# Performance work log

Hardware: AMD Instinct MI355X
Metric: run time of the kernel (lower is better)

Reference implementation:

```python
import jax, jax.numpy as jnp
import numpy as np

BETA, ALPHA, NS_STEPS = 0.9, 1.0, 1
D_MODEL, D_STATE, D_CONV, EXPAND = 768, 16, 4, 2
D_INNER = EXPAND * D_MODEL
DT_RANK = -(-D_MODEL // 16)  # ceil(d_model/16) = 48
B, L = 2, 1024


def setup_inputs() -> dict:
    key = jax.random.key(0)
    ks = jax.random.split(key, 8)
    s = lambda k, shape, sc=0.02: jax.random.normal(k, shape, jnp.float32) * sc
    return {
        "hidden_states": jax.random.normal(ks[0], (B, L, D_MODEL), jnp.float32),
        "in_proj_w": s(ks[1], (2 * D_INNER, D_MODEL)),
        "conv_w": s(ks[2], (D_INNER, 1, D_CONV), 0.2),
        "conv_b": jnp.zeros((D_INNER,), jnp.float32),
        "x_proj_w": s(ks[3], (DT_RANK + 2 * D_STATE, D_INNER)),
        "dt_head_w": s(ks[4], (D_INNER, DT_RANK)),
        "dt_head_b": s(ks[5], (D_INNER,), 0.1),
        "out_proj_w": s(ks[6], (D_MODEL, D_INNER)),
        "D": jnp.ones((D_INNER,), jnp.float32),
    }


def _newton_schulz(G, steps):
    """Muon-style quintic Newton-Schulz orthogonalization of (b, d, n) with d >= n."""
    a, b, c = 3.4445, -4.7750, 2.0315
    X = G / (jnp.linalg.norm(G, axis=(-2, -1), keepdims=True) + 1e-7)
    X = X.swapaxes(-2, -1)  # (b, n, d): rows <= cols
    for _ in range(steps):
        A = X @ X.swapaxes(-2, -1)       # (b, n, n) small Gram
        Bm = b * A + c * (A @ A)
        X = a * X + Bm @ X
    return X.swapaxes(-2, -1)            # back to (b, d, n)


def reference(hidden_states, in_proj_w, conv_w, conv_b, x_proj_w, dt_head_w, dt_head_b, out_proj_w, D):
    Bz, Lz, _ = hidden_states.shape
    dtype = hidden_states.dtype
    # input projection -> x, z  (B, L, d_inner) each
    xz = jnp.einsum('bld,ed->ble', hidden_states, in_proj_w)
    x, z = jnp.split(xz, 2, axis=-1)
    # causal depthwise conv over time + SiLU
    xc = jax.lax.conv_general_dilated(
        x.swapaxes(1, 2), conv_w, (1,), [(D_CONV - 1, 0)],
        dimension_numbers=('NCH', 'OIH', 'NCH'), feature_group_count=D_INNER)
    x = jax.nn.silu(xc.swapaxes(1, 2) + conv_b)  # (B, L, d_inner)
    # projections for dt / k / q
    x_dbl = jnp.einsum('bld,ed->ble', x, x_proj_w)
    dt_low, k, q = jnp.split(x_dbl, [DT_RANK, DT_RANK + D_STATE], axis=-1)
    dt = jnp.einsum('blr,dr->bld', dt_low, dt_head_w)  # (B, L, d_inner), bias applied in scan

    def step(carry, inp):
        v, h = carry  # velocity / hidden states, each (b, d_inner, d_state)
        x_t, dt_t, k_t, q_t = inp
        dt_t = jax.nn.sigmoid(dt_t + dt_head_b)                              # (b, d)
        dt_t = dt_t / (1.0 + dt_t * jnp.sum(k_t * k_t, axis=-1, keepdims=True))
        dA = 1.0 - dt_t[:, :, None] * (k_t * k_t)[:, None, :]                # (b, d, n)
        G = (dt_t * x_t)[:, :, None] * k_t[:, None, :]                       # dt * u * k
        v = BETA * v + ALPHA * _newton_schulz(G, NS_STEPS)
        h = dA * h + v
        y_t = jnp.einsum('bdn,bn->bd', h, q_t) + D * x_t
        return (v, h), y_t

    init = (jnp.zeros((Bz, D_INNER, D_STATE), dtype),
            jnp.zeros((Bz, D_INNER, D_STATE), dtype))
    xs = (x.swapaxes(0, 1), dt.swapaxes(0, 1), k.swapaxes(0, 1), q.swapaxes(0, 1))
    _, y = jax.lax.scan(step, init, xs)        # (L, B, d_inner)
    y = y.swapaxes(0, 1) * jax.nn.silu(z)      # gate
    return jnp.einsum('bld,od->blo', y, out_proj_w)
```

## Files before the change

### kernel.cpp

```cpp
#include <hip/hip_runtime.h>

#define D_MODEL 768
#define D_STATE 16
#define D_INNER 1536
#define DT_RANK 48
#define NB 2
#define LSEQ 1024
#define NROWS (NB * LSEQ)
#define CCH 32
#define CLEN (LSEQ / CCH)
#define STP 16
#define BETA_CL 3.4336838e-02f
#define OUT_ELEMS (NROWS * D_MODEL)

typedef __attribute__((ext_vector_type(4))) float f32x4;
typedef __attribute__((ext_vector_type(8))) short s16x8;
typedef __attribute__((ext_vector_type(8))) unsigned short u16x8;
typedef __attribute__((ext_vector_type(4))) unsigned short u16x4;

__device__ __forceinline__ unsigned short f2bu(float f) {
  unsigned int x = __builtin_bit_cast(unsigned int, f);
  x += 0x7fffu + ((x >> 16) & 1u);
  return (unsigned short)(x >> 16);
}

typedef __attribute__((address_space(3))) unsigned int as3u32;
typedef __attribute__((address_space(1))) const unsigned int as1u32;
__device__ __forceinline__ void gload16(const unsigned short* g, unsigned short* l) {
  __builtin_amdgcn_global_load_lds((as1u32*)g, (as3u32*)l, 16, 0, 0);
}

#define CVT_TOTAL 663552
#define Z1_GROUPS 20480
#define Z2_GROUPS 256
__global__ __launch_bounds__(256) void cvt5z_kernel(const float* __restrict__ s0,
                                                    const float* __restrict__ s1,
                                                    const float* __restrict__ s2,
                                                    const float* __restrict__ s3,
                                                    const float* __restrict__ s4,
                                                    unsigned short* __restrict__ d0,
                                                    unsigned short* __restrict__ d1,
                                                    unsigned short* __restrict__ d2,
                                                    unsigned short* __restrict__ d3,
                                                    unsigned short* __restrict__ d4,
                                                    float* __restrict__ z1,
                                                    float* __restrict__ z2) {
  int g = blockIdx.x * 256 + threadIdx.x;
  if (g >= CVT_TOTAL) {
    int zg = g - CVT_TOTAL;
    f32x4 zero = {0.f, 0.f, 0.f, 0.f};
    if (zg < Z1_GROUPS) {
      *(f32x4*)(z1 + zg * 8) = zero;
      *(f32x4*)(z1 + zg * 8 + 4) = zero;
    } else if (zg < Z1_GROUPS + Z2_GROUPS) {
      int i = (zg - Z1_GROUPS) * 8;
      *(f32x4*)(z2 + i) = zero;
      *(f32x4*)(z2 + i + 4) = zero;
    }
    return;
  }
  const float* s;
  unsigned short* d;
  int base;
  if (g < 196608)      { s = s0; d = d0; base = 0; }
  else if (g < 491520) { s = s1; d = d1; base = 196608; }
  else if (g < 506880) { s = s2; d = d2; base = 491520; }
  else if (g < 516096) { s = s3; d = d3; base = 506880; }
  else                 { s = s4; d = d4; base = 516096; }
  int i = (g - base) * 8;
  f32x4 a = *(const f32x4*)(s + i);
  f32x4 b = *(const f32x4*)(s + i + 4);
  u16x8 o;
#pragma unroll
  for (int j = 0; j < 4; j++) { o[j] = f2bu(a[j]); o[4 + j] = f2bu(b[j]); }
  *(u16x8*)(d + i) = o;
}

template <bool PARTIAL>
__global__ __launch_bounds__(256) void gemm128(const unsigned short* __restrict__ A,
                                               const unsigned short* __restrict__ B,
                                               float* __restrict__ C, int K,
                                               int lda, int ldb, int ldc, int kseg_len) {
  __shared__ __align__(16) unsigned short As[2][128 * 32];
  __shared__ __align__(16) unsigned short Bs[2][128 * 32];
  const int m0 = blockIdx.y * 128, n0 = blockIdx.x * 128;
  const int kbeg = blockIdx.z * kseg_len;
  const int kend = kbeg + kseg_len;
  const int t = threadIdx.x;
  const int wave = t >> 6, lane = t & 63;
  const int wm = wave >> 1, wn = wave & 1;
  const int quad = lane >> 4, l16 = lane & 15;
  const int srow = lane >> 2;
  const int kcol = (lane & 3) * 8;

  float* Cp = C;
  if constexpr (PARTIAL) Cp = C + (size_t)blockIdx.z * (size_t)gridDim.y * 128 * ldc;

  auto stage = [&](int bi, int k0) {
#pragma unroll
    for (int r = 0; r < 2; r++) {
      const int seg = r * 64 + wave * 16;
      gload16(A + (size_t)(m0 + seg + srow) * lda + k0 + kcol, &As[bi][seg * 32]);
      gload16(B + (size_t)(n0 + seg + srow) * ldb + k0 + kcol, &Bs[bi][seg * 32]);
    }
  };

  f32x4 acc[4][4] = {};
  stage(0, kbeg);
  __syncthreads();
  int buf = 0;
  for (int k0 = kbeg; k0 < kend; k0 += 32) {
    if (k0 + 32 < kend) stage(buf ^ 1, k0 + 32);
    s16x8 af[4], bf[4];
#pragma unroll
    for (int i = 0; i < 4; i++) {
      af[i] = *(const s16x8*)&As[buf][(wm * 64 + i * 16 + l16) * 32 + quad * 8];
      bf[i] = *(const s16x8*)&Bs[buf][(wn * 64 + i * 16 + l16) * 32 + quad * 8];
    }
#pragma unroll
    for (int mi = 0; mi < 4; mi++)
#pragma unroll
      for (int ni = 0; ni < 4; ni++)
        acc[mi][ni] = __builtin_amdgcn_mfma_f32_16x16x32_bf16(af[mi], bf[ni], acc[mi][ni], 0, 0, 0);
    __syncthreads();
    buf ^= 1;
  }
#pragma unroll
  for (int mi = 0; mi < 4; mi++)
#pragma unroll
    for (int ni = 0; ni < 4; ni++)
#pragma unroll
      for (int r = 0; r < 4; r++) {
        int row = m0 + wm * 64 + mi * 16 + quad * 4 + r;
        int col = n0 + wn * 64 + ni * 16 + l16;
        Cp[(size_t)row * ldc + col] = acc[mi][ni][r];
      }
}

__global__ __launch_bounds__(256) void reduce4_kernel(const float* __restrict__ part,
                                                      float* __restrict__ out) {
  int i4 = (blockIdx.x * 256 + threadIdx.x) * 4;
  f32x4 a = *(const f32x4*)(part + i4);
  f32x4 b = *(const f32x4*)(part + (size_t)OUT_ELEMS + i4);
  f32x4 c = *(const f32x4*)(part + (size_t)2 * OUT_ELEMS + i4);
  f32x4 d = *(const f32x4*)(part + (size_t)3 * OUT_ELEMS + i4);
  f32x4 o;
#pragma unroll
  for (int j = 0; j < 4; j++) o[j] = (a[j] + b[j]) + (c[j] + d[j]);
  *(f32x4*)(out + i4) = o;
}

template <bool AF32, bool ATOMIC, bool DTF>
__global__ __launch_bounds__(256) void gemm_bt(const void* __restrict__ Av,
                                               const unsigned short* __restrict__ B,
                                               float* __restrict__ C, int M, int N, int K,
                                               int lda, int ldb, int ldc, int kseg_len,
                                               const float* __restrict__ dtb,
                                               const float* __restrict__ xconv,
                                               float* __restrict__ nubuf) {
  __shared__ __align__(16) unsigned short As[2][64][40];
  __shared__ __align__(16) unsigned short Bs[2][64][40];
  __shared__ float nk_s[64];
  const int m0 = blockIdx.y * 64, n0 = blockIdx.x * 64;
  const int kbeg = blockIdx.z * kseg_len;
  const int kend = (kbeg + kseg_len < K) ? (kbeg + kseg_len) : K;
  const int t = threadIdx.x;
  const int wave = t >> 6, lane = t & 63;
  const int wm = wave >> 1, wn = wave & 1;
  const int quad = lane >> 4, l16 = lane & 15;
  const int srow = t >> 2;
  const int kseg = (t & 3) * 8;
  const bool va = (m0 + srow) < M, vb = (n0 + srow) < N;
  const float* Af = (const float*)Av;
  const unsigned short* Ab = (const unsigned short*)Av;
  const unsigned short* Bp = B + (size_t)(n0 + srow) * ldb;

  f32x4 ra0, ra1;
  u16x8 rab, rbb;
  auto pref = [&](int k0) {
    const int kk = k0 + kseg;
    const int krem = kend - kk;
    if constexpr (AF32) {
      const float* Ap = Af + (size_t)(m0 + srow) * lda + kk;
      if (va && krem >= 8) {
        ra0 = *(const f32x4*)Ap;
        ra1 = *(const f32x4*)(Ap + 4);
      } else {
#pragma unroll
        for (int j = 0; j < 4; j++) {
          ra0[j] = (va && j < krem) ? Ap[j] : 0.0f;
          ra1[j] = (va && j + 4 < krem) ? Ap[j + 4] : 0.0f;
        }
      }
    } else {
      const unsigned short* Ap = Ab + (size_t)(m0 + srow) * lda + kk;
      if (va && krem >= 8) {
        rab = *(const u16x8*)Ap;
      } else {
#pragma unroll
        for (int j = 0; j < 8; j++) rab[j] = (va && j < krem) ? Ap[j] : (unsigned short)0;
      }
    }
    if (vb && krem >= 8) {
      rbb = *(const u16x8*)(Bp + kk);
    } else {
#pragma unroll
      for (int j = 0; j < 8; j++) rbb[j] = (vb && j < krem) ? Bp[kk + j] : (unsigned short)0;
    }
  };
  auto tolds = [&](int bi) {
    if constexpr (AF32) {
      u16x8 oa;
#pragma unroll
      for (int j = 0; j < 4; j++) { oa[j] = f2bu(ra0[j]); oa[4 + j] = f2bu(ra1[j]); }
      *(u16x8*)&As[bi][srow][kseg] = oa;
    } else {
      *(u16x8*)&As[bi][srow][kseg] = rab;
    }
    *(u16x8*)&Bs[bi][srow][kseg] = rbb;
  };

  f32x4 acc[2][2] = {};
  pref(kbeg);
  tolds(0);
  if constexpr (DTF) {
    if (t < 64 && (m0 + t) < M) {
      const float* kr = Af + (size_t)(m0 + t) * lda + 48;
      float nk = 0.0f;
#pragma unroll
      for (int n = 0; n < 16; n++) nk += kr[n] * kr[n];
      nk_s[t] = nk;
    }
  }
  __syncthreads();
  int buf = 0;
  for (int k0 = kbeg; k0 < kend; k0 += 32) {
    const bool more = (k0 + 32 < kend);
    if (more) pref(k0 + 32);
    s16x8 a0 = *(const s16x8*)&As[buf][wm * 32 + l16][quad * 8];
    s16x8 a1 = *(const s16x8*)&As[buf][wm * 32 + 16 + l16][quad * 8];
    s16x8 b0 = *(const s16x8*)&Bs[buf][wn * 32 + l16][quad * 8];
    s16x8 b1 = *(const s16x8*)&Bs[buf][wn * 32 + 16 + l16][quad * 8];
    acc[0][0] = __builtin_amdgcn_mfma_f32_16x16x32_bf16(a0, b0, acc[0][0], 0, 0, 0);
    acc[0][1] = __builtin_amdgcn_mfma_f32_16x16x32_bf16(a0, b1, acc[0][1], 0, 0, 0);
    acc[1][0] = __builtin_amdgcn_mfma_f32_16x16x32_bf16(a1, b0, acc[1][0], 0, 0, 0);
    acc[1][1] = __builtin_amdgcn_mfma_f32_16x16x32_bf16(a1, b1, acc[1][1], 0, 0, 0);
    if (more) tolds(buf ^ 1);
    __syncthreads();
    buf ^= 1;
  }
  if constexpr (DTF) {
    float u2[2][4] = {};
#pragma unroll
    for (int mi = 0; mi < 2; mi++)
#pragma unroll
      for (int ni = 0; ni < 2; ni++)
#pragma unroll
        for (int r = 0; r < 4; r++) {
          int row = m0 + wm * 32 + mi * 16 + quad * 4 + r;
          int col = n0 + wn * 32 + ni * 16 + l16;
          float sg = 1.0f / (1.0f + expf(-(acc[mi][ni][r] + dtb[col])));
          float dv = sg / (1.0f + sg * nk_s[row - m0]);
          C[(size_t)row * ldc + col] = dv;
          float u = dv * xconv[(size_t)row * D_INNER + col];
          u2[mi][r] += u * u;
        }
#pragma unroll
    for (int mi = 0; mi < 2; mi++)
#pragma unroll
      for (int r = 0; r < 4; r++) {
        float v = u2[mi][r];
        v += __shfl_xor(v, 1);
        v += __shfl_xor(v, 2);
        v += __shfl_xor(v, 4);
        v += __shfl_xor(v, 8);
        if (l16 == 0)
          atomicAdd(&nubuf[m0 + wm * 32 + mi * 16 + quad * 4 + r], v);
      }
  } else {
#pragma unroll
    for (int mi = 0; mi < 2; mi++)
#pragma unroll
      for (int ni = 0; ni < 2; ni++)
#pragma unroll
        for (int r = 0; r < 4; r++) {
          int row = m0 + wm * 32 + mi * 16 + quad * 4 + r;
          int col = n0 + wn * 32 + ni * 16 + l16;
          if (row < M && col < N) {
            if constexpr (ATOMIC)
              atomicAdd(&C[(size_t)row * ldc + col], acc[mi][ni][r]);
            else
              C[(size_t)row * ldc + col] = acc[mi][ni][r];
          }
        }
  }
}

__global__ __launch_bounds__(256) void conv_silu_kernel(const float* __restrict__ xz,
                                                        const float* __restrict__ cw,
                                                        const float* __restrict__ cb,
                                                        float* __restrict__ xc,
                                                        unsigned short* __restrict__ xcb) {
  int g = blockIdx.x * 256 + threadIdx.x;
  int c4 = (g % 384) * 4;
  int row = g / 384;
  int l = row & (LSEQ - 1);
  f32x4 acc = *(const f32x4*)(cb + c4);
  f32x4 w[4];
#pragma unroll
  for (int ci = 0; ci < 4; ci++) w[ci] = *(const f32x4*)(cw + (c4 + ci) * 4);
#pragma unroll
  for (int j = 0; j < 4; j++) {
    int dl = l - 3 + j;
    if (dl >= 0) {
      f32x4 xv = *(const f32x4*)(xz + (size_t)(row - 3 + j) * 3072 + c4);
#pragma unroll
      for (int ci = 0; ci < 4; ci++) acc[ci] = fmaf(xv[ci], w[ci][j], acc[ci]);
    }
  }
  f32x4 val;
  u16x4 ob;
#pragma unroll
  for (int ci = 0; ci < 4; ci++) {
    float sg = 1.0f / (1.0f + expf(-acc[ci]));
    val[ci] = acc[ci] * sg;
    ob[ci] = f2bu(val[ci]);
  }
  *(f32x4*)(xc + (size_t)row * D_INNER + c4) = val;
  *(u16x4*)(xcb + (size_t)row * D_INNER + c4) = ob;
}

__device__ __forceinline__ float gamma_of(float nu, float nk) {
  float p = nu * nk;
  float s = sqrtf(p) + 1e-7f;
  float tt = p / (s * s);
  return (3.4445f + tt * (-4.7750f + 2.0315f * tt)) / s;
}

__global__ __launch_bounds__(256) void scan_phase1(const float* __restrict__ xconv,
                                                   const float* __restrict__ dtbuf,
                                                   const float* __restrict__ xdbl,
                                                   const float* __restrict__ nubuf,
                                                   float* __restrict__ cvp,
                                                   float* __restrict__ chp,
                                                   float* __restrict__ gp,
                                                   float* __restrict__ rp) {
  __shared__ __align__(16) float xc_s[2][STP][64];
  __shared__ __align__(16) float dt_s[2][STP][64];
  __shared__ __align__(16) float kq_s[2][STP][36];
  __shared__ float g_s[2][STP];
  const int t = threadIdx.x;
  const int nq = t & 3, dloc = t >> 2;
  const int b = blockIdx.x / (24 * CCH);
  const int rem = blockIdx.x % (24 * CCH);
  const int d0 = (rem / CCH) * 64;
  const int c = rem % CCH;
  const int tbase = c * CLEN;
  const size_t ub = ((size_t)b * LSEQ + tbase) * D_INNER + d0;
  const float* kqb = xdbl + ((size_t)b * LSEQ + tbase) * 80 + 48;
  const float* nub = nubuf + (size_t)b * LSEQ + tbase;
  const int prow = t >> 4, pcol = (t & 15) * 4;
  const int krow = t >> 3, kcol = (t & 7) * 4;
  f32x4 pxc, pd, pk;
  float pg;
  auto prefetch = [&](int t0) {
    size_t off = ub + (size_t)(t0 + prow) * D_INNER + pcol;
    pxc = *(const f32x4*)(xconv + off);
    pd = *(const f32x4*)(dtbuf + off);
    if (t < 128) pk = *(const f32x4*)(kqb + (size_t)(t0 + krow) * 80 + kcol);
    if (t < STP) {
      const float* kr = kqb + (size_t)(t0 + t) * 80;
      float nk = 0.0f;
#pragma unroll
      for (int n = 0; n < 16; n++) nk += kr[n] * kr[n];
      pg = gamma_of(nub[t0 + t], nk);
    }
  };
  auto writelds = [&](int bi) {
    *(f32x4*)&xc_s[bi][prow][pcol] = pxc;
    *(f32x4*)&dt_s[bi][prow][pcol] = pd;
    if (t < 128) *(f32x4*)&kq_s[bi][krow][kcol] = pk;
    if (t < STP) g_s[bi][t] = pg;
  };
  f32x4 v = {0.f, 0.f, 0.f, 0.f}, h = {0.f, 0.f, 0.f, 0.f};
  f32x4 g = {0.f, 0.f, 0.f, 0.f}, r = {1.f, 1.f, 1.f, 1.f};
  float bt = 0.9f;
  prefetch(0);
  writelds(0);
  __syncthreads();
  int buf = 0;
  for (int t0 = 0; t0 < CLEN; t0 += STP) {
    const bool more = (t0 + STP < CLEN);
    if (more) prefetch(t0 + STP);
#pragma unroll 4
    for (int s = 0; s < STP; s++) {
      float dtf = dt_s[buf][s][dloc];
      float u = g_s[buf][s] * dtf * xc_s[buf][s][dloc];
#pragma unroll
      for (int j = 0; j < 4; j++) {
        float kj = kq_s[buf][s][nq * 4 + j];
        v[j] = fmaf(0.9f, v[j], u * kj);
        float a = fmaf(-dtf * kj, kj, 1.0f);
        h[j] = fmaf(a, h[j], v[j]);
        r[j] *= a;
        g[j] = fmaf(a, g[j], bt);
      }
      bt *= 0.9f;
    }
    if (more) writelds(buf ^ 1);
    __syncthreads();
    buf ^= 1;
  }
  size_t o = (((size_t)b * CCH + c) * D_INNER + d0 + dloc) * 16 + nq * 4;
  *(f32x4*)(cvp + o) = v;
  *(f32x4*)(chp + o) = h;
  *(f32x4*)(gp + o) = g;
  *(f32x4*)(rp + o) = r;
}

__global__ __launch_bounds__(256) void scan_phase2(const float* __restrict__ cvp,
                                                   const float* __restrict__ chp,
                                                   float* __restrict__ gp,
                                                   float* __restrict__ rp) {
  int i = blockIdx.x * 256 + threadIdx.x;
  int b = i / (D_INNER * 16);
  int rem = i % (D_INNER * 16);
  float v0 = 0.f, h0 = 0.f;
#pragma unroll
  for (int c = 0; c < CCH; c++) {
    size_t o = ((size_t)(b * CCH + c)) * (D_INNER * 16) + rem;
    float cv = cvp[o], ch = chp[o], gg = gp[o], rr = rp[o];
    gp[o] = v0;
    rp[o] = h0;
    float v0n = fmaf(BETA_CL, v0, cv);
    float h0n = fmaf(gg, v0, fmaf(rr, h0, ch));
    v0 = v0n;
    h0 = h0n;
  }
}

__global__ __launch_bounds__(256) void scan_phase3(const float* __restrict__ dtbuf,
                                                   const float* __restrict__ xdbl,
                                                   const float* __restrict__ nubuf,
                                                   const float* __restrict__ gp,
                                                   const float* __restrict__ rp,
                                                   const float* __restrict__ xconv,
                                                   const float* __restrict__ xz,
                                                   const float* __restrict__ Dp,
                                                   unsigned short* __restrict__ ygb) {
  __shared__ __align__(16) float xc_s[2][STP][64];
  __shared__ __align__(16) float dt_s[2][STP][64];
  __shared__ __align__(16) float z_s[2][STP][64];
  __shared__ __align__(16) float kq_s[2][STP][36];
  __shared__ float g_s[2][STP];
  const int t = threadIdx.x;
  const int nq = t & 3, dloc = t >> 2;
  const int b = blockIdx.x / (24 * CCH);
  const int rem = blockIdx.x % (24 * CCH);
  const int d0 = (rem / CCH) * 64;
  const int c = rem % CCH;
  const int tbase = c * CLEN;
  const size_t ub = ((size_t)b * LSEQ + tbase) * D_INNER + d0;
  const float* kqb = xdbl + ((size_t)b * LSEQ + tbase) * 80 + 48;
  const float* nub = nubuf + (size_t)b * LSEQ + tbase;
  const float* z0 = xz + ((size_t)b * LSEQ + tbase) * 3072 + 1536 + d0;
  unsigned short* y_p = ygb + (size_t)b * LSEQ * D_INNER + d0 + dloc;
  const int prow = t >> 4, pcol = (t & 15) * 4;
  const int krow = t >> 3, kcol = (t & 7) * 4;
  f32x4 pxc, pd, pz, pk;
  float pg;
  auto prefetch = [&](int t0) {
    size_t off = ub + (size_t)(t0 + prow) * D_INNER + pcol;
    pxc = *(const f32x4*)(xconv + off);
    pd = *(const f32x4*)(dtbuf + off);
    pz = *(const f32x4*)(z0 + (size_t)(t0 + prow) * 3072 + pcol);
    if (t < 128) pk = *(const f32x4*)(kqb + (size_t)(t0 + krow) * 80 + kcol);
    if (t < STP) {
      const float* kr = kqb + (size_t)(t0 + t) * 80;
      float nk = 0.0f;
#pragma unroll
      for (int n = 0; n < 16; n++) nk += kr[n] * kr[n];
      pg = gamma_of(nub[t0 + t], nk);
    }
  };
  auto writelds = [&](int bi) {
    *(f32x4*)&xc_s[bi][prow][pcol] = pxc;
    *(f32x4*)&dt_s[bi][prow][pcol] = pd;
    *(f32x4*)&z_s[bi][prow][pcol] = pz;
    if (t < 128) *(f32x4*)&kq_s[bi][krow][kcol] = pk;
    if (t < STP) g_s[bi][t] = pg;
  };
  size_t so = (((size_t)b * CCH + c) * D_INNER + d0 + dloc) * 16 + nq * 4;
  f32x4 v = *(const f32x4*)(gp + so);
  f32x4 h = *(const f32x4*)(rp + so);
  const float Dd = Dp[d0 + dloc];
  prefetch(0);
  writelds(0);
  __syncthreads();
  int buf = 0;
  for (int t0 = 0; t0 < CLEN; t0 += STP) {
    const bool more = (t0 + STP < CLEN);
    if (more) prefetch(t0 + STP);
#pragma unroll 4
    for (int s = 0; s < STP; s++) {
      float xcv = xc_s[buf][s][dloc];
      float dtf = dt_s[buf][s][dloc];
      float u = g_s[buf][s] * dtf * xcv;
      f32x4 kv = *(const f32x4*)&kq_s[buf][s][nq * 4];
      f32x4 qv = *(const f32x4*)&kq_s[buf][s][16 + nq * 4];
      float yp = 0.0f;
#pragma unroll
      for (int j = 0; j < 4; j++) {
        float kj = kv[j];
        v[j] = fmaf(0.9f, v[j], u * kj);
        float dA = fmaf(-dtf * kj, kj, 1.0f);
        h[j] = fmaf(dA, h[j], v[j]);
        yp = fmaf(h[j], qv[j], yp);
      }
      yp += __shfl_xor(yp, 1);
      yp += __shfl_xor(yp, 2);
      float zv = z_s[buf][s][dloc];
      float sz = zv / (1.0f + expf(-zv));
      float val = (yp + Dd * xcv) * sz;
      if (nq == 0) y_p[(size_t)(tbase + t0 + s) * D_INNER] = f2bu(val);
    }
    if (more) writelds(buf ^ 1);
    __syncthreads();
    buf ^= 1;
  }
}

extern "C" void kernel_launch(void* const* d_in, const int* in_sizes, int n_in,
                              void* d_out, int out_size, void* d_ws, size_t ws_size,
                              hipStream_t stream) {
  const float* hidden = (const float*)d_in[0];
  const float* w_in   = (const float*)d_in[1];
  const float* conv_w = (const float*)d_in[2];
  const float* conv_b = (const float*)d_in[3];
  const float* w_x    = (const float*)d_in[4];
  const float* w_dt   = (const float*)d_in[5];
  const float* b_dt   = (const float*)d_in[6];
  const float* w_out  = (const float*)d_in[7];
  const float* Dp     = (const float*)d_in[8];

  float* ws    = (float*)d_ws;
  float* xz    = ws;
  float* xconv = xz + (size_t)NROWS * 3072;
  float* xdbl  = xconv + (size_t)NROWS * D_INNER;
  float* dtbuf = xdbl + (size_t)NROWS * 80;
  float* nubuf = dtbuf + (size_t)NROWS * D_INNER;
  const size_t PL = (size_t)NB * CCH * D_INNER * 16;
  float* cvp   = nubuf + NROWS;
  float* chp   = cvp + PL;
  float* gp    = chp + PL;
  float* rp    = gp + PL;
  float* opart = rp + PL;
  unsigned short* bfr = (unsigned short*)(opart + (size_t)4 * OUT_ELEMS);
  unsigned short* hbf = bfr;
  unsigned short* wib = hbf + 1572864;
  unsigned short* wxb = wib + 2359296;
  unsigned short* wdb = wxb + 122880;
  unsigned short* wob = wdb + 73728;
  unsigned short* xcb = wob + 1179648;
  unsigned short* ygb = xcb + 3145728;

  dim3 blk(256);
  cvt5z_kernel<<<dim3((CVT_TOTAL + Z1_GROUPS + Z2_GROUPS) / 256), blk, 0, stream>>>(
      hidden, w_in, w_x, w_dt, w_out, hbf, wib, wxb, wdb, wob, xdbl, nubuf);
  gemm128<false><<<dim3(24, 16, 1), blk, 0, stream>>>(hbf, wib, xz, 768, 768, 768, 3072, 768);
  conv_silu_kernel<<<dim3(3072), blk, 0, stream>>>(xz, conv_w, conv_b, xconv, xcb);
  gemm_bt<false, true, false><<<dim3(2, 32, 8), blk, 0, stream>>>(
      xcb, wxb, xdbl, 2048, 80, 1536, 1536, 1536, 80, 192, nullptr, nullptr, nullptr);
  gemm_bt<true, false, true><<<dim3(24, 32, 1), blk, 0, stream>>>(
      xdbl, wdb, dtbuf, 2048, 1536, 48, 80, 48, 1536, 48, b_dt, xconv, nubuf);
  scan_phase1<<<dim3(NB * 24 * CCH), blk, 0, stream>>>(xconv, dtbuf, xdbl, nubuf,
                                                       cvp, chp, gp, rp);
  scan_phase2<<<dim3(192), blk, 0, stream>>>(cvp, chp, gp, rp);
  scan_phase3<<<dim3(NB * 24 * CCH), blk, 0, stream>>>(dtbuf, xdbl, nubuf, gp, rp,
                                                       xconv, xz, Dp, ygb);
  gemm128<true><<<dim3(6, 16, 4), blk, 0, stream>>>(ygb, wob, opart, 1536,
                                                    1536, 1536, 768, 384);
  reduce4_kernel<<<dim3(OUT_ELEMS / 1024), blk, 0, stream>>>(opart, (float*)d_out);
}
```

Baseline: 207.0 us.

## Fuse three chunked-scan phases into one cooperative kernel with grid syncs

Merges the per-chunk local scan, the cross-chunk carry propagation and the output scan into a single cooperative kernel separated by grid-wide syncs. Each block keeps its whole chunk of xconv, dt and k/q in LDS, so the second pass no longer reloads them from global memory. Chunk count drops from 32 to 16 so the grid of 768 blocks can be co-resident, with launch bounds set for 3 blocks per CU. The cost is two grid barriers, less parallelism per chunk in the sequential loops, and the loss of the earlier double-buffered prefetch overlap.

```diff
diff --git a/kernel.cpp b/kernel.cpp
--- a/kernel.cpp
+++ b/kernel.cpp
@@ -1,4 +1,6 @@
 #include <hip/hip_runtime.h>
+#include <hip/hip_cooperative_groups.h>
+namespace cg = cooperative_groups;
 
 #define D_MODEL 768
 #define D_STATE 16
@@ -7,10 +9,9 @@
 #define NB 2
 #define LSEQ 1024
 #define NROWS (NB * LSEQ)
-#define CCH 32
+#define CCH 16
 #define CLEN (LSEQ / CCH)
-#define STP 16
-#define BETA_CL 3.4336838e-02f
+#define BETA_CL 1.1790185e-03f
 #define OUT_ELEMS (NROWS * D_MODEL)
 
 typedef __attribute__((ext_vector_type(4))) float f32x4;
@@ -337,122 +338,21 @@
   return (3.4445f + tt * (-4.7750f + 2.0315f * tt)) / s;
 }
 
-__global__ __launch_bounds__(256) void scan_phase1(const float* __restrict__ xconv,
-                                                   const float* __restrict__ dtbuf,
-                                                   const float* __restrict__ xdbl,
-                                                   const float* __restrict__ nubuf,
-                                                   float* __restrict__ cvp,
-                                                   float* __restrict__ chp,
-                                                   float* __restrict__ gp,
-                                                   float* __restrict__ rp) {
-  __shared__ __align__(16) float xc_s[2][STP][64];
-  __shared__ __align__(16) float dt_s[2][STP][64];
-  __shared__ __align__(16) float kq_s[2][STP][36];
-  __shared__ float g_s[2][STP];
-  const int t = threadIdx.x;
-  const int nq = t & 3, dloc = t >> 2;
-  const int b = blockIdx.x / (24 * CCH);
-  const int rem = blockIdx.x % (24 * CCH);
-  const int d0 = (rem / CCH) * 64;
-  const int c = rem % CCH;
-  const int tbase = c * CLEN;
-  const size_t ub = ((size_t)b * LSEQ + tbase) * D_INNER + d0;
-  const float* kqb = xdbl + ((size_t)b * LSEQ + tbase) * 80 + 48;
-  const float* nub = nubuf + (size_t)b * LSEQ + tbase;
-  const int prow = t >> 4, pcol = (t & 15) * 4;
-  const int krow = t >> 3, kcol = (t & 7) * 4;
-  f32x4 pxc, pd, pk;
-  float pg;
-  auto prefetch = [&](int t0) {
-    size_t off = ub + (size_t)(t0 + prow) * D_INNER + pcol;
-    pxc = *(const f32x4*)(xconv + off);
-    pd = *(const f32x4*)(dtbuf + off);
-    if (t < 128) pk = *(const f32x4*)(kqb + (size_t)(t0 + krow) * 80 + kcol);
-    if (t < STP) {
-      const float* kr = kqb + (size_t)(t0 + t) * 80;
-      float nk = 0.0f;
-#pragma unroll
-      for (int n = 0; n < 16; n++) nk += kr[n] * kr[n];
-      pg = gamma_of(nub[t0 + t], nk);
-    }
-  };
-  auto writelds = [&](int bi) {
-    *(f32x4*)&xc_s[bi][prow][pcol] = pxc;
-    *(f32x4*)&dt_s[bi][prow][pcol] = pd;
-    if (t < 128) *(f32x4*)&kq_s[bi][krow][kcol] = pk;
-    if (t < STP) g_s[bi][t] = pg;
-  };
-  f32x4 v = {0.f, 0.f, 0.f, 0.f}, h = {0.f, 0.f, 0.f, 0.f};
-  f32x4 g = {0.f, 0.f, 0.f, 0.f}, r = {1.f, 1.f, 1.f, 1.f};
-  float bt = 0.9f;
-  prefetch(0);
-  writelds(0);
-  __syncthreads();
-  int buf = 0;
-  for (int t0 = 0; t0 < CLEN; t0 += STP) {
-    const bool more = (t0 + STP < CLEN);
-    if (more) prefetch(t0 + STP);
-#pragma unroll 4
-    for (int s = 0; s < STP; s++) {
-      float dtf = dt_s[buf][s][dloc];
-      float u = g_s[buf][s] * dtf * xc_s[buf][s][dloc];
-#pragma unroll
-      for (int j = 0; j < 4; j++) {
-        float kj = kq_s[buf][s][nq * 4 + j];
-        v[j] = fmaf(0.9f, v[j], u * kj);
-        float a = fmaf(-dtf * kj, kj, 1.0f);
-        h[j] = fmaf(a, h[j], v[j]);
-        r[j] *= a;
-        g[j] = fmaf(a, g[j], bt);
-      }
-      bt *= 0.9f;
-    }
-    if (more) writelds(buf ^ 1);
-    __syncthreads();
-    buf ^= 1;
-  }
-  size_t o = (((size_t)b * CCH + c) * D_INNER + d0 + dloc) * 16 + nq * 4;
-  *(f32x4*)(cvp + o) = v;
-  *(f32x4*)(chp + o) = h;
-  *(f32x4*)(gp + o) = g;
-  *(f32x4*)(rp + o) = r;
-}
-
-__global__ __launch_bounds__(256) void scan_phase2(const float* __restrict__ cvp,
-                                                   const float* __restrict__ chp,
-                                                   float* __restrict__ gp,
-                                                   float* __restrict__ rp) {
-  int i = blockIdx.x * 256 + threadIdx.x;
-  int b = i / (D_INNER * 16);
-  int rem = i % (D_INNER * 16);
-  float v0 = 0.f, h0 = 0.f;
-#pragma unroll
-  for (int c = 0; c < CCH; c++) {
-    size_t o = ((size_t)(b * CCH + c)) * (D_INNER * 16) + rem;
-    float cv = cvp[o], ch = chp[o], gg = gp[o], rr = rp[o];
-    gp[o] = v0;
-    rp[o] = h0;
-    float v0n = fmaf(BETA_CL, v0, cv);
-    float h0n = fmaf(gg, v0, fmaf(rr, h0, ch));
-    v0 = v0n;
-    h0 = h0n;
-  }
-}
-
-__global__ __launch_bounds__(256) void scan_phase3(const float* __restrict__ dtbuf,
-                                                   const float* __restrict__ xdbl,
-                                                   const float* __restrict__ nubuf,
-                                                   const float* __restrict__ gp,
-                                                   const float* __restrict__ rp,
-                                                   const float* __restrict__ xconv,
-                                                   const float* __restrict__ xz,
-                                                   const float* __restrict__ Dp,
-                                                   unsigned short* __restrict__ ygb) {
-  __shared__ __align__(16) float xc_s[2][STP][64];
-  __shared__ __align__(16) float dt_s[2][STP][64];
-  __shared__ __align__(16) float z_s[2][STP][64];
-  __shared__ __align__(16) float kq_s[2][STP][36];
-  __shared__ float g_s[2][STP];
+__global__ __launch_bounds__(256, 3) void scan_fused(const float* __restrict__ xconv,
+                                                     const float* __restrict__ dtbuf,
+                                                     const float* __restrict__ xdbl,
+                                                     const float* __restrict__ nubuf,
+                                                     const float* __restrict__ xz,
+                                                     const float* __restrict__ Dp,
+                                                     float* __restrict__ cvp,
+                                                     float* __restrict__ chp,
+                                                     float* __restrict__ gp,
+                                                     float* __restrict__ rp,
+                                                     unsigned short* __restrict__ ygb) {
+  __shared__ __align__(16) float xc_s[CLEN][64];
+  __shared__ __align__(16) float dt_s[CLEN][64];
+  __shared__ __align__(16) float kq_s[CLEN][36];
+  __shared__ float g_s[CLEN];
   const int t = threadIdx.x;
   const int nq = t & 3, dloc = t >> 2;
   const int b = blockIdx.x / (24 * CCH);
@@ -467,66 +367,98 @@
   unsigned short* y_p = ygb + (size_t)b * LSEQ * D_INNER + d0 + dloc;
   const int prow = t >> 4, pcol = (t & 15) * 4;
   const int krow = t >> 3, kcol = (t & 7) * 4;
-  f32x4 pxc, pd, pz, pk;
-  float pg;
-  auto prefetch = [&](int t0) {
-    size_t off = ub + (size_t)(t0 + prow) * D_INNER + pcol;
-    pxc = *(const f32x4*)(xconv + off);
-    pd = *(const f32x4*)(dtbuf + off);
-    pz = *(const f32x4*)(z0 + (size_t)(t0 + prow) * 3072 + pcol);
-    if (t < 128) pk = *(const f32x4*)(kqb + (size_t)(t0 + krow) * 80 + kcol);
-    if (t < STP) {
-      const float* kr = kqb + (size_t)(t0 + t) * 80;
-      float nk = 0.0f;
-#pragma unroll
-      for (int n = 0; n < 16; n++) nk += kr[n] * kr[n];
-      pg = gamma_of(nub[t0 + t], nk);
-    }
-  };
-  auto writelds = [&](int bi) {
-    *(f32x4*)&xc_s[bi][prow][pcol] = pxc;
-    *(f32x4*)&dt_s[bi][prow][pcol] = pd;
-    *(f32x4*)&z_s[bi][prow][pcol] = pz;
-    if (t < 128) *(f32x4*)&kq_s[bi][krow][kcol] = pk;
-    if (t < STP) g_s[bi][t] = pg;
-  };
-  size_t so = (((size_t)b * CCH + c) * D_INNER + d0 + dloc) * 16 + nq * 4;
-  f32x4 v = *(const f32x4*)(gp + so);
-  f32x4 h = *(const f32x4*)(rp + so);
+
+#pragma unroll
+  for (int i = 0; i < 4; i++) {
+    int row = prow + 16 * i;
+    size_t off = ub + (size_t)row * D_INNER + pcol;
+    *(f32x4*)&xc_s[row][pcol] = *(const f32x4*)(xconv + off);
+    *(f32x4*)&dt_s[row][pcol] = *(const f32x4*)(dtbuf + off);
+  }
+#pragma unroll
+  for (int i = 0; i < 2; i++) {
+    int row = krow + 32 * i;
+    *(f32x4*)&kq_s[row][kcol] = *(const f32x4*)(kqb + (size_t)row * 80 + kcol);
+  }
+  __syncthreads();
+  if (t < CLEN) {
+    float nk = 0.0f;
+#pragma unroll
+    for (int n = 0; n < 16; n++) nk += kq_s[t][n] * kq_s[t][n];
+    g_s[t] = gamma_of(nub[t], nk);
+  }
+  __syncthreads();
+
+  f32x4 v = {0.f, 0.f, 0.f, 0.f}, h = {0.f, 0.f, 0.f, 0.f};
+  f32x4 g = {0.f, 0.f, 0.f, 0.f}, r = {1.f, 1.f, 1.f, 1.f};
+  float bt = 0.9f;
+#pragma unroll 4
+  for (int s = 0; s < CLEN; s++) {
+    float dtf = dt_s[s][dloc];
+    float u = g_s[s] * dtf * xc_s[s][dloc];
+#pragma unroll
+    for (int j = 0; j < 4; j++) {
+      float kj = kq_s[s][nq * 4 + j];
+      v[j] = fmaf(0.9f, v[j], u * kj);
+      float a = fmaf(-dtf * kj, kj, 1.0f);
+      h[j] = fmaf(a, h[j], v[j]);
+      r[j] *= a;
+      g[j] = fmaf(a, g[j], bt);
+    }
+    bt *= 0.9f;
+  }
+  size_t o = (((size_t)b * CCH + c) * D_INNER + d0 + dloc) * 16 + nq * 4;
+  *(f32x4*)(cvp + o) = v;
+  *(f32x4*)(chp + o) = h;
+  *(f32x4*)(gp + o) = g;
+  *(f32x4*)(rp + o) = r;
+
+  cg::this_grid().sync();
+
+  int gid = blockIdx.x * 256 + t;
+  if (gid < NB * D_INNER * 16) {
+    int bb = gid / (D_INNER * 16);
+    int rm = gid % (D_INNER * 16);
+    float v0 = 0.f, h0 = 0.f;
+#pragma unroll
+    for (int cc = 0; cc < CCH; cc++) {
+      size_t oo = ((size_t)(bb * CCH + cc)) * (D_INNER * 16) + rm;
+      float cv = cvp[oo], ch = chp[oo], gg = gp[oo], rr = rp[oo];
+      gp[oo] = v0;
+      rp[oo] = h0;
+      float v0n = fmaf(BETA_CL, v0, cv);
+      float h0n = fmaf(gg, v0, fmaf(rr, h0, ch));
+      v0 = v0n;
+      h0 = h0n;
+    }
+  }
+
+  cg::this_grid().sync();
+
+  v = *(const f32x4*)(gp + o);
+  h = *(const f32x4*)(rp + o);
   const float Dd = Dp[d0 + dloc];
-  prefetch(0);
-  writelds(0);
-  __syncthreads();
-  int buf = 0;
-  for (int t0 = 0; t0 < CLEN; t0 += STP) {
-    const bool more = (t0 + STP < CLEN);
-    if (more) prefetch(t0 + STP);
 #pragma unroll 4
-    for (int s = 0; s < STP; s++) {
-      float xcv = xc_s[buf][s][dloc];
-      float dtf = dt_s[buf][s][dloc];
-      float u = g_s[buf][s] * dtf * xcv;
-      f32x4 kv = *(const f32x4*)&kq_s[buf][s][nq * 4];
-      f32x4 qv = *(const f32x4*)&kq_s[buf][s][16 + nq * 4];
-      float yp = 0.0f;
-#pragma unroll
-      for (int j = 0; j < 4; j++) {
-        float kj = kv[j];
-        v[j] = fmaf(0.9f, v[j], u * kj);
-        float dA = fmaf(-dtf * kj, kj, 1.0f);
-        h[j] = fmaf(dA, h[j], v[j]);
-        yp = fmaf(h[j], qv[j], yp);
-      }
-      yp += __shfl_xor(yp, 1);
-      yp += __shfl_xor(yp, 2);
-      float zv = z_s[buf][s][dloc];
+  for (int s = 0; s < CLEN; s++) {
+    float xcv = xc_s[s][dloc];
+    float dtf = dt_s[s][dloc];
+    float u = g_s[s] * dtf * xcv;
+    float yp = 0.0f;
+#pragma unroll
+    for (int j = 0; j < 4; j++) {
+      float kj = kq_s[s][nq * 4 + j];
+      v[j] = fmaf(0.9f, v[j], u * kj);
+      float dA = fmaf(-dtf * kj, kj, 1.0f);
+      h[j] = fmaf(dA, h[j], v[j]);
+      yp = fmaf(h[j], kq_s[s][16 + nq * 4 + j], yp);
+    }
+    yp += __shfl_xor(yp, 1);
+    yp += __shfl_xor(yp, 2);
+    if (nq == 0) {
+      float zv = z0[(size_t)s * 3072 + dloc];
       float sz = zv / (1.0f + expf(-zv));
-      float val = (yp + Dd * xcv) * sz;
-      if (nq == 0) y_p[(size_t)(tbase + t0 + s) * D_INNER] = f2bu(val);
-    }
-    if (more) writelds(buf ^ 1);
-    __syncthreads();
-    buf ^= 1;
+      y_p[(size_t)(tbase + s) * D_INNER] = f2bu((yp + Dd * xcv) * sz);
+    }
   }
 }
 
@@ -573,11 +505,13 @@
       xcb, wxb, xdbl, 2048, 80, 1536, 1536, 1536, 80, 192, nullptr, nullptr, nullptr);
   gemm_bt<true, false, true><<<dim3(24, 32, 1), blk, 0, stream>>>(
       xdbl, wdb, dtbuf, 2048, 1536, 48, 80, 48, 1536, 48, b_dt, xconv, nubuf);
-  scan_phase1<<<dim3(NB * 24 * CCH), blk, 0, stream>>>(xconv, dtbuf, xdbl, nubuf,
-                                                       cvp, chp, gp, rp);
-  scan_phase2<<<dim3(192), blk, 0, stream>>>(cvp, chp, gp, rp);
-  scan_phase3<<<dim3(NB * 24 * CCH), blk, 0, stream>>>(dtbuf, xdbl, nubuf, gp, rp,
-                                                       xconv, xz, Dp, ygb);
+  {
+    void* sargs[] = {(void*)&xconv, (void*)&dtbuf, (void*)&xdbl, (void*)&nubuf,
+                     (void*)&xz, (void*)&Dp, (void*)&cvp, (void*)&chp,
+                     (void*)&gp, (void*)&rp, (void*)&ygb};
+    hipLaunchCooperativeKernel((void*)scan_fused, dim3(NB * 24 * CCH), blk,
+                               sargs, 0, stream);
+  }
   gemm128<true><<<dim3(6, 16, 4), blk, 0, stream>>>(ygb, wob, opart, 1536,
                                                     1536, 1536, 768, 384);
   reduce4_kernel<<<dim3(OUT_ELEMS / 1024), blk, 0, stream>>>(opart, (float*)d_out);
```

After: 377.9 us. 1.83x slower.
